# Performance work log

Hardware: AMD Instinct MI355X
Metric: run time of the kernel (lower is better)

## Reference

```python
import jax, jax.numpy as jnp
import numpy as np
import math

D_MODEL = 512
KEY_DIM = 128
NUM_LAYERS = 2
TEMP = 30.0
NORM_EPS = 1e-5
NORM_SCALE = math.sqrt(1.0 / (D_MODEL * 4 * 4))


def _l2norm_lastdim(x):
    # F.normalize(x, p=2, dim=-1): x / max(||x||, 1e-12)
    n = jnp.sqrt(jnp.sum(x * x, axis=-1, keepdims=True))
    return x / jnp.maximum(n, 1e-12)


def _attn(q, k, v, WK, bK):
    # q: [Sq,B,D], k: [Sk,B,D], v: [Sk,B,D] -> [Sq,B,D]
    wq = _l2norm_lastdim(q @ WK + bK)            # [Sq,B,K]
    wk = _l2norm_lastdim(k @ WK + bK)            # [Sk,B,K]
    dot = jnp.einsum('qbk,sbk->bqs', wq, wk)     # cosine sims
    aff = jax.nn.softmax(dot * TEMP, axis=-1)
    return jnp.einsum('bqs,sbd->qbd', aff, v)


def _instance_norm(x, h, w):
    # x: [HW,B,D]; InstanceL2Norm over (D,h,w) per batch element, size_average=True
    HW, B, D = x.shape
    ss = jnp.sum(x * x, axis=(0, 2))             # [B]
    factor = NORM_SCALE * jnp.sqrt((D * h * w) / (ss + NORM_EPS))
    return x * factor[None, :, None]


def _encoder(src4d, WKs, bKs):
    B, D, H, W = src4d.shape
    x = src4d.reshape(B, D, H * W).transpose(2, 0, 1)   # [HW,B,D]
    for _ in range(NUM_LAYERS):
        x = _instance_norm(x + _attn(x, x, x, WKs, bKs), H, W)
    return x  # memory [HW,B,D]


def _decoder(tgt4d, memory, pos, WKs, bKs, WKc, bKc):
    B, D, H, W = tgt4d.shape
    x = tgt4d.reshape(B, D, H * W).transpose(2, 0, 1)   # [HW,B,D]
    for _ in range(NUM_LAYERS):
        x = _instance_norm(x + _attn(x, x, x, WKs, bKs), H, W)
        mask = _attn(x, memory, pos, WKc, bKc)
        t2 = _instance_norm(x * mask, H, W)
        t3 = _attn(x, memory, memory * pos, WKc, bKc)
        t4 = _instance_norm(x + t3, H, W)
        x = _instance_norm(t2 + t4, H, W)
    feat = x.reshape(H, W, B, D).transpose(2, 3, 0, 1)  # [B,D,H,W]
    return feat


def setup_inputs() -> dict:
    key = jax.random.key(0)
    k1, k2, k3, k4, k5 = jax.random.split(key, 5)
    B, D, H, W = 16, D_MODEL, 32, 32
    std = math.sqrt(2.0 / KEY_DIM)
    return {
        'train_feat': jax.random.normal(k1, (B, D, H, W), jnp.float32),
        'test_feat': jax.random.normal(k2, (B, D, H, W), jnp.float32),
        'train_label': jax.random.uniform(k3, (B, H, W), jnp.float32),
        'WK_self': jax.random.normal(k4, (D, KEY_DIM), jnp.float32) * std,
        'bK_self': jnp.zeros((KEY_DIM,), jnp.float32),
        'WK_cross': jax.random.normal(k5, (D, KEY_DIM), jnp.float32) * std,
        'bK_cross': jnp.zeros((KEY_DIM,), jnp.float32),
    }


def reference(train_feat, test_feat, train_label, WK_self, bK_self, WK_cross, bK_cross):
    B, D, H, W = train_feat.shape
    memory = _encoder(train_feat, WK_self, bK_self)              # [HW,B,D]
    # pos: label [B,H,W] -> [HW,B,1] -> broadcast to [HW,B,D]
    pos = jnp.broadcast_to(train_label.reshape(B, H * W).T[:, :, None], (H * W, B, D))
    encoded_feat = _decoder(train_feat, memory, pos, WK_self, bK_self, WK_cross, bK_cross)
    decoded_feat = _decoder(test_feat, memory, pos, WK_self, bK_self, WK_cross, bK_cross)
    return (encoded_feat, decoded_feat)
```

## Files before the change

### kernel.cpp

```cpp
#include <hip/hip_runtime.h>
#include <math.h>

#define NB 16
#define SEQ 1024
#define DM 512
#define KD 128
#define TEMP_F 30.0f
#define NS_F 0.011048543456039805f
#define DS_F 524288.0f

#define SS_IDX(grp, b) (((grp) * NB + (b)) * 16)
#define SS_STRIDE 768
#define SS_STAGES 12
#define SS_FLOATS (SS_STRIDE * SS_STAGES)

typedef short bf16x8 __attribute__((ext_vector_type(8)));
typedef float f32x4 __attribute__((ext_vector_type(4)));
typedef unsigned short us;
typedef unsigned short us8 __attribute__((ext_vector_type(8)));

__device__ __forceinline__ us f2bf(float x) {
    union { float f; unsigned u; } v; v.f = x;
    unsigned r = v.u + 0x7fffu + ((v.u >> 16) & 1u);
    return (us)(r >> 16);
}
__device__ __forceinline__ float bf2f(us h) {
    union { unsigned u; float f; } v; v.u = ((unsigned)h) << 16;
    return v.f;
}

#define GLL16(gp, lp) __builtin_amdgcn_global_load_lds( \
    (__attribute__((address_space(1))) void*)(unsigned long long)(gp), \
    (__attribute__((address_space(3))) void*)(unsigned)(unsigned long long)(lp), 16, 0, 0)


__global__ __launch_bounds__(256) void k_transpose_in(const float* __restrict__ src,
                                                      us* __restrict__ XC,
                                                      us* __restrict__ XT) {
    __shared__ float tile[32][33];
    const int b = blockIdx.z;
    const int d0 = blockIdx.x * 32;
    const int s0 = blockIdx.y * 32;
    const int tx = threadIdx.x, ty = threadIdx.y;
    const float* p = src + (size_t)b * DM * SEQ;
    us* pt = XT + (size_t)b * DM * SEQ;
    us* pc = XC + (size_t)b * SEQ * 1024;
#pragma unroll
    for (int j = 0; j < 32; j += 8) {
        const size_t o = (size_t)(d0 + ty + j) * SEQ + s0 + tx;
        const float v = p[o];
        tile[ty + j][tx] = v;
        pt[o] = f2bf(v);
    }
    __syncthreads();
#pragma unroll
    for (int j = 0; j < 4; ++j) {
        const int s = s0 + ty + j * 8;
        const int d = d0 + tx;
        const float v = tile[tx][ty + j * 8];
        const us h = f2bf(v);
        pc[(size_t)s * 1024 + d] = h;
        pc[(size_t)s * 1024 + 512 + d] = f2bf(v - bf2f(h));
    }
}

__global__ __launch_bounds__(256) void k_mklabel(const us* __restrict__ MT,
                                                 const float* __restrict__ label,
                                                 us* __restrict__ ML) {
    const int b = blockIdx.y;
    const size_t off = ((size_t)blockIdx.x * 256 + threadIdx.x) * 8;
    const int s = (int)(off & (SEQ - 1));
    const size_t o = (size_t)b * DM * SEQ + off;
    us8 v = *(const us8*)(MT + o);
    const float4 l0 = *(const float4*)(label + (size_t)b * SEQ + s);
    const float4 l1 = *(const float4*)(label + (size_t)b * SEQ + s + 4);
    us8 r;
    r[0] = f2bf(bf2f(v[0]) * l0.x); r[1] = f2bf(bf2f(v[1]) * l0.y);
    r[2] = f2bf(bf2f(v[2]) * l0.z); r[3] = f2bf(bf2f(v[3]) * l0.w);
    r[4] = f2bf(bf2f(v[4]) * l1.x); r[5] = f2bf(bf2f(v[5]) * l1.y);
    r[6] = f2bf(bf2f(v[6]) * l1.z); r[7] = f2bf(bf2f(v[7]) * l1.w);
    *(us8*)(ML + o) = r;
}

__global__ __launch_bounds__(256) void k_wsplit(const float* __restrict__ WK,
                                                us* __restrict__ WC) {
    const int k = blockIdx.x;
    for (int d = threadIdx.x; d < DM; d += 256) {
        const float v = WK[(size_t)d * KD + k];
        const us h = f2bf(v);
        WC[(size_t)k * 1024 + d] = h;
        WC[(size_t)k * 1024 + 512 + d] = f2bf(v - bf2f(h));
    }
}

__global__ __launch_bounds__(256) void k_proj(const us* __restrict__ XC,
                                              const us* __restrict__ WC,
                                              const float* __restrict__ bK,
                                              us* __restrict__ Wout) {
    const int row0 = blockIdx.x * 32;
    __shared__ short As[32 * 64], Bs[128 * 64];
    __shared__ float ssp[2][32];
    const int tid = threadIdx.x, w = tid >> 6, l = tid & 63;
    const int wm = (w >> 1) * 16, wn = (w & 1) * 64;
    const int sr = l >> 3, sc = (((l & 7) ^ (l >> 3)) << 3);
    const int lr = l & 15, lk = (l >> 4) * 8;
    const int sx = (lr & 7) << 3;
    f32x4 acc[4] = {};
    for (int k0 = 0; k0 < 1536; k0 += 64) {
        const int ak0 = (k0 < 1024) ? k0 : k0 - 1024;
        const int bk0 = (k0 < 512) ? k0 : k0 - 512;
        GLL16(XC + (size_t)(row0 + w * 8 + sr) * 1024 + ak0 + sc, &As[w * 512]);
#pragma unroll
        for (int cc = 0; cc < 4; ++cc) {
            const int c = 4 * w + cc;
            GLL16(WC + (size_t)(c * 8 + sr) * 1024 + bk0 + sc, &Bs[c * 512]);
        }
        __syncthreads();
#pragma unroll
        for (int kc = 0; kc < 2; ++kc) {
            const int kk = kc * 32 + lk;
            const bf16x8 a = *(const bf16x8*)&As[(wm + lr) * 64 + (kk ^ sx)];
            bf16x8 bb[4];
#pragma unroll
            for (int fn = 0; fn < 4; ++fn)
                bb[fn] = *(const bf16x8*)&Bs[(wn + fn * 16 + lr) * 64 + (kk ^ sx)];
#pragma unroll
            for (int fn = 0; fn < 4; ++fn)
                acc[fn] = __builtin_amdgcn_mfma_f32_16x16x32_bf16(a, bb[fn], acc[fn], 0, 0, 0);
        }
        __syncthreads();
    }
    const int er = l & 15, eq = (l >> 4) * 4;
    const int nh = w & 1;
    float bkv[4];
#pragma unroll
    for (int fn = 0; fn < 4; ++fn) bkv[fn] = bK[wn + fn * 16 + er];
    float vv[4][4];
#pragma unroll
    for (int r = 0; r < 4; ++r) {
        float ss = 0.f;
#pragma unroll
        for (int fn = 0; fn < 4; ++fn) {
            const float t = acc[fn][r] + bkv[fn];
            vv[fn][r] = t;
            ss += t * t;
        }
#pragma unroll
        for (int o = 8; o > 0; o >>= 1) ss += __shfl_xor(ss, o, 64);
        if (er == 0) ssp[nh][wm + eq + r] = ss;
    }
    __syncthreads();
#pragma unroll
    for (int r = 0; r < 4; ++r) {
        const int rowloc = wm + eq + r;
        const float tot = ssp[0][rowloc] + ssp[1][rowloc];
        const float invn = 1.0f / fmaxf(sqrtf(tot), 1e-12f);
        const size_t ro = (size_t)(row0 + rowloc) * 256;
#pragma unroll
        for (int fn = 0; fn < 4; ++fn) {
            const float ov = vv[fn][r] * invn;
            const us h = f2bf(ov);
            Wout[ro + wn + fn * 16 + er] = h;
            Wout[ro + 128 + wn + fn * 16 + er] = f2bf(ov - bf2f(h));
        }
    }
}

__global__ __launch_bounds__(256) void k_qk(const us* __restrict__ Qc,
                                            const us* __restrict__ Kc,
                                            const float* __restrict__ labelp,
                                            us* __restrict__ P,
                                            float* __restrict__ RS,
                                            float* __restrict__ RL, int b0) {
    const int flat = blockIdx.x + (int)gridDim.x * (blockIdx.y + (int)gridDim.y * blockIdx.z);
    const int chunk = ((int)gridDim.x * (int)gridDim.y * (int)gridDim.z) >> 3;
    const int logical = (flat & 7) * chunk + (flat >> 3);
    const int jx = logical & 7;
    const int iy = (logical >> 3) & 7;
    const int bz = logical >> 6;
    const int b = b0 + bz;
    const int i0 = iy * 128, j0 = jx * 128;
    const int jb = jx;
    const us* Ab = Qc + (size_t)b * SEQ * 256;
    const us* Bb = Kc + (size_t)b * SEQ * 256;
    __shared__ short As[128 * 64], Bs[128 * 64];
    __shared__ float shrs[2][128], shrl[2][128];
    const int tid = threadIdx.x, w = tid >> 6, l = tid & 63;
    const int wm = (w >> 1) * 64, wn = (w & 1) * 64;
    const int sr = l >> 3, sc = (((l & 7) ^ (l >> 3)) << 3);
    const int lr = l & 15, lk = (l >> 4) * 8;
    const int sx = (lr & 7) << 3;
    f32x4 acc[4][4] = {};
    for (int k0 = 0; k0 < 384; k0 += 64) {
        const int ak0 = (k0 < 256) ? k0 : k0 - 256;
        const int bk0 = (k0 < 128) ? k0 : k0 - 128;
#pragma unroll
        for (int cc = 0; cc < 4; ++cc) {
            const int c = 4 * w + cc;
            GLL16(Ab + (size_t)(i0 + c * 8 + sr) * 256 + ak0 + sc, &As[c * 512]);
            GLL16(Bb + (size_t)(j0 + c * 8 + sr) * 256 + bk0 + sc, &Bs[c * 512]);
        }
        __syncthreads();
#pragma unroll
        for (int kc = 0; kc < 2; ++kc) {
            const int kk = kc * 32 + lk;
            bf16x8 a[4], bb[4];
#pragma unroll
            for (int f = 0; f < 4; ++f) {
                a[f]  = *(const bf16x8*)&As[(wm + f * 16 + lr) * 64 + (kk ^ sx)];
                bb[f] = *(const bf16x8*)&Bs[(wn + f * 16 + lr) * 64 + (kk ^ sx)];
            }
#pragma unroll
            for (int fm = 0; fm < 4; ++fm)
#pragma unroll
                for (int fn = 0; fn < 4; ++fn)
                    acc[fm][fn] = __builtin_amdgcn_mfma_f32_16x16x32_bf16(a[fm], bb[fn], acc[fm][fn], 0, 0, 0);
        }
        __syncthreads();
    }
    us* Pb = P + (size_t)bz * SEQ * SEQ;
    const int er = l & 15, eq = (l >> 4) * 4;
    float lb[4] = {0.f, 0.f, 0.f, 0.f};
    if (labelp) {
#pragma unroll
        for (int fn = 0; fn < 4; ++fn) lb[fn] = labelp[(size_t)b * SEQ + j0 + wn + fn * 16 + er];
    }
#pragma unroll
    for (int fm = 0; fm < 4; ++fm)
#pragma unroll
        for (int r = 0; r < 4; ++r) {
            float s = 0.f, sl = 0.f;
#pragma unroll
            for (int fn = 0; fn < 4; ++fn) {
                const float e = __expf(fmaf(TEMP_F, acc[fm][fn][r], -TEMP_F));
                Pb[(size_t)(i0 + wm + fm * 16 + eq + r) * SEQ + j0 + wn + fn * 16 + er] = f2bf(e);
                s += e;
                sl += e * lb[fn];
            }
#pragma unroll
            for (int o = 1; o < 16; o <<= 1) {
                s += __shfl_xor(s, o, 64);
                sl += __shfl_xor(sl, o, 64);
            }
            if (er == 0) {
                shrs[w & 1][wm + fm * 16 + eq + r] = s;
                shrl[w & 1][wm + fm * 16 + eq + r] = sl;
            }
        }
    __syncthreads();
    if (tid < 128) {
        const size_t o = ((size_t)b * 8 + jb) * SEQ + i0 + tid;
        RS[o] = shrs[0][tid] + shrs[1][tid];
        if (labelp) RL[o] = shrl[0][tid] + shrl[1][tid];
    }
}

__global__ __launch_bounds__(256) void k_pv(const us* __restrict__ P,
                                            const us* __restrict__ VT,
                                            const us* __restrict__ XC,
                                            const float* __restrict__ RS,
                                            const float* __restrict__ RL,
                                            float* __restrict__ MVEC,
                                            float* __restrict__ Cout,
                                            float* __restrict__ SS, int b0, int mode) {
    const int flat = blockIdx.x + (int)gridDim.x * (blockIdx.y + (int)gridDim.y * blockIdx.z);
    const int chunk = ((int)gridDim.x * (int)gridDim.y * (int)gridDim.z) >> 3;
    const int logical = (flat & 7) * chunk + (flat >> 3);
    const int jx = logical & 3;
    const int iy = (logical >> 2) & 15;
    const int bz = logical >> 6;
    const int b = b0 + bz;
    const int i0 = iy * 64, j0 = jx * 128;
    const us* Pb = P + (size_t)bz * SEQ * SEQ;
    const us* Vb = VT + (size_t)b * DM * SEQ;
    __shared__ short As[64 * 64], Bs[128 * 64];
    __shared__ float sh_inv[64], sh_m[64];
    __shared__ float ps[3][4];
    const int tid = threadIdx.x, w = tid >> 6, l = tid & 63;
    const int wm = (w >> 1) * 32, wn = (w & 1) * 64;
    const int sr = l >> 3, sc = (((l & 7) ^ (l >> 3)) << 3);
    const int lr = l & 15, lk = (l >> 4) * 8;
    const int sx = (lr & 7) << 3;
    f32x4 acc[2][4] = {};
    for (int k0 = 0; k0 < SEQ; k0 += 64) {
#pragma unroll
        for (int cc = 0; cc < 2; ++cc) {
            const int c = 2 * w + cc;
            GLL16(Pb + (size_t)(i0 + c * 8 + sr) * SEQ + k0 + sc, &As[c * 512]);
        }
#pragma unroll
        for (int cc = 0; cc < 4; ++cc) {
            const int c = 4 * w + cc;
            GLL16(Vb + (size_t)(j0 + c * 8 + sr) * SEQ + k0 + sc, &Bs[c * 512]);
        }
        __syncthreads();
#pragma unroll
        for (int kc = 0; kc < 2; ++kc) {
            const int kk = kc * 32 + lk;
            bf16x8 a[2], bb[4];
#pragma unroll
            for (int fm = 0; fm < 2; ++fm)
                a[fm] = *(const bf16x8*)&As[(wm + fm * 16 + lr) * 64 + (kk ^ sx)];
#pragma unroll
            for (int fn = 0; fn < 4; ++fn)
                bb[fn] = *(const bf16x8*)&Bs[(wn + fn * 16 + lr) * 64 + (kk ^ sx)];
#pragma unroll
            for (int fm = 0; fm < 2; ++fm)
#pragma unroll
                for (int fn = 0; fn < 4; ++fn)
                    acc[fm][fn] = __builtin_amdgcn_mfma_f32_16x16x32_bf16(a[fm], bb[fn], acc[fm][fn], 0, 0, 0);
        }
        __syncthreads();
    }
    if (tid < 64) {
        const size_t base = (size_t)b * 8 * SEQ + i0 + tid;
        float s = 0.f;
#pragma unroll
        for (int jb = 0; jb < 8; ++jb) s += RS[base + (size_t)jb * SEQ];
        const float inv = 1.0f / s;
        sh_inv[tid] = inv;
        if (mode == 2) {
            float sl = 0.f;
#pragma unroll
            for (int jb = 0; jb < 8; ++jb) sl += RL[base + (size_t)jb * SEQ];
            const float mv = sl * inv;
            sh_m[tid] = mv;
            if (jx == 0) MVEC[(size_t)b * SEQ + i0 + tid] = mv;
        }
    }
    __syncthreads();
    const us* XCb = XC + (size_t)b * SEQ * 1024;
    float sa = 0.f, sb = 0.f, sab = 0.f;
    const int er = l & 15, eq = (l >> 4) * 4;
#pragma unroll
    for (int fm = 0; fm < 2; ++fm)
#pragma unroll
        for (int fn = 0; fn < 4; ++fn)
#pragma unroll
            for (int r = 0; r < 4; ++r) {
                const int lrow = wm + fm * 16 + eq + r;
                const int col = j0 + wn + fn * 16 + er;
                float v = acc[fm][fn][r] * sh_inv[lrow];
                const size_t o = ((size_t)b * SEQ + i0 + lrow) * DM + col;
                const size_t xo = (size_t)(i0 + lrow) * 1024 + col;
                const float x = bf2f(XCb[xo]) + bf2f(XCb[xo + 512]);
                v += x;
                sb += v * v;
                if (mode == 2) {
                    const float a = x * sh_m[lrow];
                    sa += a * a;
                    sab += a * v;
                }
                Cout[o] = v;
            }
#pragma unroll
    for (int off = 32; off > 0; off >>= 1) {
        sb += __shfl_xor(sb, off, 64);
        if (mode == 2) { sa += __shfl_xor(sa, off, 64); sab += __shfl_xor(sab, off, 64); }
    }
    if (l == 0) { ps[0][w] = sb; ps[1][w] = sa; ps[2][w] = sab; }
    __syncthreads();
    if (tid == 0) {
        if (mode == 1) {
            atomicAdd(&SS[SS_IDX(0, b)], ps[0][0] + ps[0][1] + ps[0][2] + ps[0][3]);
        } else {
            atomicAdd(&SS[SS_IDX(0, b)], ps[1][0] + ps[1][1] + ps[1][2] + ps[1][3]);
            atomicAdd(&SS[SS_IDX(1, b)], ps[0][0] + ps[0][1] + ps[0][2] + ps[0][3]);
            atomicAdd(&SS[SS_IDX(2, b)], ps[2][0] + ps[2][1] + ps[2][2] + ps[2][3]);
        }
    }
}

__global__ void k_zero(float* __restrict__ SSb) {
    const int i = blockIdx.x * 256 + threadIdx.x;
    if (i < SS_FLOATS) SSb[i] = 0.0f;
}

__global__ __launch_bounds__(256) void k_finish(const float* __restrict__ Tin,
                                                const us* __restrict__ XCin,
                                                const float* __restrict__ mv,
                                                const float* __restrict__ SS,
                                                us* __restrict__ XCout,
                                                us* __restrict__ XTb,
                                                float* __restrict__ XTf,
                                                int mode, int writeXC) {
    const int b = blockIdx.z;
    const int s0 = blockIdx.x * 32, d0 = blockIdx.y * 32;
    const int tx = threadIdx.x, ty = threadIdx.y;
    __shared__ float tile[32][33];
    float f1 = 0.f, f2 = 0.f, f3;
    if (mode == 0) {
        f3 = NS_F * sqrtf(DS_F / (SS[SS_IDX(0, b)] + 1e-5f));
    } else {
        const float ssa = SS[SS_IDX(0, b)], ssb = SS[SS_IDX(1, b)], ssab = SS[SS_IDX(2, b)];
        f1 = NS_F * sqrtf(DS_F / (ssa + 1e-5f));
        f2 = NS_F * sqrtf(DS_F / (ssb + 1e-5f));
        const float ssc = f1 * f1 * ssa + 2.f * f1 * f2 * ssab + f2 * f2 * ssb;
        f3 = NS_F * sqrtf(DS_F / (ssc + 1e-5f));
    }
#pragma unroll
    for (int j = 0; j < 4; ++j) {
        const int s = s0 + ty + j * 8;
        const int d = d0 + tx;
        const size_t o = ((size_t)b * SEQ + s) * DM + d;
        const size_t xo = ((size_t)b * SEQ + s) * 1024 + d;
        float v;
        if (mode == 0) v = f3 * Tin[o];
        else {
            const float x = bf2f(XCin[xo]) + bf2f(XCin[xo + 512]);
            v = f3 * (f1 * x * mv[(size_t)b * SEQ + s] + f2 * Tin[o]);
        }
        if (writeXC) {
            const us h = f2bf(v);
            XCout[xo] = h;
            XCout[xo + 512] = f2bf(v - bf2f(h));
        }
        tile[ty + j * 8][tx] = v;
    }
    __syncthreads();
#pragma unroll
    for (int j = 0; j < 4; ++j) {
        const int d = d0 + ty + j * 8;
        const int s = s0 + tx;
        const float v = tile[tx][ty + j * 8];
        const size_t o = ((size_t)b * DM + d) * SEQ + s;
        if (XTb) XTb[o] = f2bf(v);
        else if (XTf) XTf[o] = v;
    }
}

extern "C" void kernel_launch(void* const* d_in, const int* in_sizes, int n_in,
                              void* d_out, int out_size, void* d_ws, size_t ws_size,
                              hipStream_t stream) {
    const float* train_feat = (const float*)d_in[0];
    const float* test_feat  = (const float*)d_in[1];
    const float* label      = (const float*)d_in[2];
    const float* WKs        = (const float*)d_in[3];
    const float* bKs        = (const float*)d_in[4];
    const float* WKc        = (const float*)d_in[5];
    const float* bKc        = (const float*)d_in[6];
    float* out = (float*)d_out;
    float* w = (float*)d_ws;

    const size_t SBD = (size_t)NB * SEQ * DM;
    const size_t SBK = (size_t)NB * SEQ * KD;

    float* T   = w;
    us* XC     = (us*)(T + SBD);
    us* XTd    = XC + 2 * SBD;
    us* MEMT   = XTd + SBD;
    us* MEMLT  = MEMT + SBD;
    us* W1C    = MEMLT + SBD;
    us* WKMC   = W1C + 2 * SBK;
    us* WCs    = WKMC + 2 * SBK;
    us* WCc    = WCs + (size_t)KD * 1024;
    float* MVEC = (float*)(WCc + (size_t)KD * 1024);
    float* SS   = MVEC + (size_t)NB * SEQ;
    float* RS   = SS + SS_FLOATS;
    float* RL   = RS + (size_t)NB * 8 * SEQ;
    float* Pf   = RL + (size_t)NB * 8 * SEQ;

    const size_t fixed = (size_t)(Pf - w);
    const size_t per = (size_t)SEQ * SEQ / 2;
    const size_t wsf = ws_size / 4;
    int cap = 1;
    if (wsf > fixed) {
        size_t c = (wsf - fixed) / per;
        if (c < 1) c = 1;
        if (c > NB) c = NB;
        cap = (int)c;
    }
    us* Pbuf = (us*)Pf;

    const dim3 gT_in(DM / 32, SEQ / 32, NB), bT(32, 8);
    const dim3 gFin(SEQ / 32, DM / 32, NB);

    int stage = 0;
    auto nextSS = [&]() { return SS + (size_t)(stage++) * SS_STRIDE; };

    auto attn = [&](const us* Qc, const us* Kc, const us* VT,
                    const float* labelp, int pvmode, float* SSst) {
        for (int b0 = 0; b0 < NB; b0 += cap) {
            const int nb = (NB - b0 < cap) ? NB - b0 : cap;
            k_qk<<<dim3(8, 8, nb), 256, 0, stream>>>(Qc, Kc, labelp, Pbuf, RS, RL, b0);
            k_pv<<<dim3(4, 16, nb), 256, 0, stream>>>(Pbuf, VT, XC, RS, RL, MVEC, T, SSst, b0, pvmode);
        }
    };

    k_zero<<<(SS_FLOATS + 255) / 256, 256, 0, stream>>>(SS);
    k_wsplit<<<KD, 256, 0, stream>>>(WKs, WCs);
    k_wsplit<<<KD, 256, 0, stream>>>(WKc, WCc);

    k_transpose_in<<<gT_in, bT, 0, stream>>>(train_feat, XC, MEMT);
    for (int l = 0; l < 2; ++l) {
        float* SSst = nextSS();
        k_proj<<<NB * SEQ / 32, 256, 0, stream>>>(XC, WCs, bKs, W1C);
        attn(W1C, W1C, MEMT, nullptr, 1, SSst);
        k_finish<<<gFin, bT, 0, stream>>>(T, XC, nullptr, SSst, XC, MEMT, nullptr, 0, 1);
    }
    k_proj<<<NB * SEQ / 32, 256, 0, stream>>>(XC, WCc, bKc, WKMC);
    k_mklabel<<<dim3(DM * SEQ / 8 / 256, NB), 256, 0, stream>>>(MEMT, label, MEMLT);

    auto decoder = [&](const float* feat, float* outp) {
        k_transpose_in<<<gT_in, bT, 0, stream>>>(feat, XC, XTd);
        for (int l = 0; l < 2; ++l) {
            float* SSst = nextSS();
            k_proj<<<NB * SEQ / 32, 256, 0, stream>>>(XC, WCs, bKs, W1C);
            attn(W1C, W1C, XTd, nullptr, 1, SSst);
            k_finish<<<gFin, bT, 0, stream>>>(T, XC, nullptr, SSst, XC, XTd, nullptr, 0, 1);
            float* SSst2 = nextSS();
            k_proj<<<NB * SEQ / 32, 256, 0, stream>>>(XC, WCc, bKc, W1C);
            attn(W1C, WKMC, MEMLT, label, 2, SSst2);
            if (l == 0)
                k_finish<<<gFin, bT, 0, stream>>>(T, XC, MVEC, SSst2, XC, XTd, nullptr, 1, 1);
            else
                k_finish<<<gFin, bT, 0, stream>>>(T, XC, MVEC, SSst2, XC, nullptr, outp, 1, 0);
        }
    };
    decoder(train_feat, out);
    decoder(test_feat, out + SBD);
}
```

Baseline: 1.013 ms.

## Fuse QK softmax and PV into single flash-style attention kernel

Replaces the two-kernel attention (QK writing a bf16 probability matrix to global memory, then PV reading it back) with one fused kernel per (batch, 64-query tile). The new kernel streams 32-key chunks of K and V through double-buffered LDS, computes exp scores, stages them in LDS as bf16 and accumulates the full 512-wide output in registers. Row sums and label sums are kept in registers, so the RS/RL buffers and batch chunking by workspace capacity go away. The intent is to remove the large P matrix round-trip through HBM and the extra launches. In exchange each block holds 128 accumulator floats per thread with occupancy of one block per CU, only 256 blocks are launched, and each block does small 32-key steps with a barrier per step.

```diff
diff --git a/kernel.cpp b/kernel.cpp
--- a/kernel.cpp
+++ b/kernel.cpp
@@ -166,193 +166,155 @@
     }
 }
 
-__global__ __launch_bounds__(256) void k_qk(const us* __restrict__ Qc,
-                                            const us* __restrict__ Kc,
-                                            const float* __restrict__ labelp,
-                                            us* __restrict__ P,
-                                            float* __restrict__ RS,
-                                            float* __restrict__ RL, int b0) {
-    const int flat = blockIdx.x + (int)gridDim.x * (blockIdx.y + (int)gridDim.y * blockIdx.z);
-    const int chunk = ((int)gridDim.x * (int)gridDim.y * (int)gridDim.z) >> 3;
-    const int logical = (flat & 7) * chunk + (flat >> 3);
-    const int jx = logical & 7;
-    const int iy = (logical >> 3) & 7;
-    const int bz = logical >> 6;
-    const int b = b0 + bz;
-    const int i0 = iy * 128, j0 = jx * 128;
-    const int jb = jx;
-    const us* Ab = Qc + (size_t)b * SEQ * 256;
-    const us* Bb = Kc + (size_t)b * SEQ * 256;
-    __shared__ short As[128 * 64], Bs[128 * 64];
-    __shared__ float shrs[2][128], shrl[2][128];
-    const int tid = threadIdx.x, w = tid >> 6, l = tid & 63;
-    const int wm = (w >> 1) * 64, wn = (w & 1) * 64;
-    const int sr = l >> 3, sc = (((l & 7) ^ (l >> 3)) << 3);
-    const int lr = l & 15, lk = (l >> 4) * 8;
-    const int sx = (lr & 7) << 3;
-    f32x4 acc[4][4] = {};
-    for (int k0 = 0; k0 < 384; k0 += 64) {
-        const int ak0 = (k0 < 256) ? k0 : k0 - 256;
-        const int bk0 = (k0 < 128) ? k0 : k0 - 128;
-#pragma unroll
-        for (int cc = 0; cc < 4; ++cc) {
-            const int c = 4 * w + cc;
-            GLL16(Ab + (size_t)(i0 + c * 8 + sr) * 256 + ak0 + sc, &As[c * 512]);
-            GLL16(Bb + (size_t)(j0 + c * 8 + sr) * 256 + bk0 + sc, &Bs[c * 512]);
-        }
-        __syncthreads();
-#pragma unroll
-        for (int kc = 0; kc < 2; ++kc) {
-            const int kk = kc * 32 + lk;
-            bf16x8 a[4], bb[4];
-#pragma unroll
-            for (int f = 0; f < 4; ++f) {
-                a[f]  = *(const bf16x8*)&As[(wm + f * 16 + lr) * 64 + (kk ^ sx)];
-                bb[f] = *(const bf16x8*)&Bs[(wn + f * 16 + lr) * 64 + (kk ^ sx)];
-            }
-#pragma unroll
-            for (int fm = 0; fm < 4; ++fm)
-#pragma unroll
-                for (int fn = 0; fn < 4; ++fn)
-                    acc[fm][fn] = __builtin_amdgcn_mfma_f32_16x16x32_bf16(a[fm], bb[fn], acc[fm][fn], 0, 0, 0);
-        }
-        __syncthreads();
-    }
-    us* Pb = P + (size_t)bz * SEQ * SEQ;
-    const int er = l & 15, eq = (l >> 4) * 4;
-    float lb[4] = {0.f, 0.f, 0.f, 0.f};
-    if (labelp) {
-#pragma unroll
-        for (int fn = 0; fn < 4; ++fn) lb[fn] = labelp[(size_t)b * SEQ + j0 + wn + fn * 16 + er];
-    }
-#pragma unroll
-    for (int fm = 0; fm < 4; ++fm)
-#pragma unroll
-        for (int r = 0; r < 4; ++r) {
-            float s = 0.f, sl = 0.f;
-#pragma unroll
-            for (int fn = 0; fn < 4; ++fn) {
-                const float e = __expf(fmaf(TEMP_F, acc[fm][fn][r], -TEMP_F));
-                Pb[(size_t)(i0 + wm + fm * 16 + eq + r) * SEQ + j0 + wn + fn * 16 + er] = f2bf(e);
-                s += e;
-                sl += e * lb[fn];
-            }
-#pragma unroll
-            for (int o = 1; o < 16; o <<= 1) {
-                s += __shfl_xor(s, o, 64);
-                sl += __shfl_xor(sl, o, 64);
-            }
-            if (er == 0) {
-                shrs[w & 1][wm + fm * 16 + eq + r] = s;
-                shrl[w & 1][wm + fm * 16 + eq + r] = sl;
-            }
-        }
-    __syncthreads();
-    if (tid < 128) {
-        const size_t o = ((size_t)b * 8 + jb) * SEQ + i0 + tid;
-        RS[o] = shrs[0][tid] + shrs[1][tid];
-        if (labelp) RL[o] = shrl[0][tid] + shrl[1][tid];
-    }
-}
-
-__global__ __launch_bounds__(256) void k_pv(const us* __restrict__ P,
-                                            const us* __restrict__ VT,
-                                            const us* __restrict__ XC,
-                                            const float* __restrict__ RS,
-                                            const float* __restrict__ RL,
-                                            float* __restrict__ MVEC,
-                                            float* __restrict__ Cout,
-                                            float* __restrict__ SS, int b0, int mode) {
-    const int flat = blockIdx.x + (int)gridDim.x * (blockIdx.y + (int)gridDim.y * blockIdx.z);
-    const int chunk = ((int)gridDim.x * (int)gridDim.y * (int)gridDim.z) >> 3;
-    const int logical = (flat & 7) * chunk + (flat >> 3);
-    const int jx = logical & 3;
-    const int iy = (logical >> 2) & 15;
-    const int bz = logical >> 6;
-    const int b = b0 + bz;
-    const int i0 = iy * 64, j0 = jx * 128;
-    const us* Pb = P + (size_t)bz * SEQ * SEQ;
-    const us* Vb = VT + (size_t)b * DM * SEQ;
-    __shared__ short As[64 * 64], Bs[128 * 64];
-    __shared__ float sh_inv[64], sh_m[64];
+__global__ __launch_bounds__(256, 1) void k_attn(const us* __restrict__ Qc,
+                                                 const us* __restrict__ Kc,
+                                                 const us* __restrict__ VT,
+                                                 const us* __restrict__ XC,
+                                                 const float* __restrict__ labelp,
+                                                 float* __restrict__ MVEC,
+                                                 float* __restrict__ Cout,
+                                                 float* __restrict__ SS, int mode) {
+    const int b = blockIdx.x;
+    const int q0 = blockIdx.y * 64;
+    __shared__ short QL[4 * 64 * 64];
+    __shared__ short KL[2][4 * 32 * 64];
+    __shared__ short VL[2][512 * 32];
+    __shared__ us PL[4 * 16 * 40];
+    __shared__ float LBL[1024];
     __shared__ float ps[3][4];
     const int tid = threadIdx.x, w = tid >> 6, l = tid & 63;
-    const int wm = (w >> 1) * 32, wn = (w & 1) * 64;
-    const int sr = l >> 3, sc = (((l & 7) ^ (l >> 3)) << 3);
+    const us* Qb = Qc + (size_t)b * SEQ * 256;
+    const us* Kb = Kc + (size_t)b * SEQ * 256;
+    const us* Vb = VT + (size_t)b * DM * SEQ;
+
+#pragma unroll
+    for (int i = 0; i < 8; ++i) {
+        const int c = w * 8 + i, rg = c >> 2, p = c & 3;
+        GLL16(Qb + (size_t)(q0 + rg * 8 + (l >> 3)) * 256 + p * 64 + (((l & 7) ^ (l >> 3)) << 3),
+              &QL[p * 4096 + rg * 512 + l * 8]);
+    }
+#pragma unroll
+    for (int i = 0; i < 1; ++i) {
+        const int c = w, rg = c >> 2, p = c & 3;
+        GLL16(Kb + (size_t)(rg * 8 + (l >> 3)) * 256 + p * 64 + (((l & 7) ^ (l >> 3)) << 3),
+              &KL[0][p * 2048 + rg * 512 + l * 8]);
+    }
+#pragma unroll
+    for (int i = 0; i < 3; ++i) {
+        const int c = 4 + w * 3 + i, rg = c >> 2, p = c & 3;
+        GLL16(Kb + (size_t)(rg * 8 + (l >> 3)) * 256 + p * 64 + (((l & 7) ^ (l >> 3)) << 3),
+              &KL[0][p * 2048 + rg * 512 + l * 8]);
+    }
+#pragma unroll
+    for (int i = 0; i < 8; ++i) {
+        const int c = w * 8 + i;
+        GLL16(Vb + (size_t)(c * 16 + (l >> 2)) * SEQ + ((((l & 3) ^ ((l >> 2) & 3))) << 3),
+              &VL[0][c * 512 + l * 8]);
+    }
+    if (labelp) {
+        GLL16(labelp + (size_t)b * SEQ + w * 256 + l * 4, &LBL[w * 256 + l * 4]);
+    }
+    __syncthreads();
+
     const int lr = l & 15, lk = (l >> 4) * 8;
-    const int sx = (lr & 7) << 3;
-    f32x4 acc[2][4] = {};
-    for (int k0 = 0; k0 < SEQ; k0 += 64) {
-#pragma unroll
-        for (int cc = 0; cc < 2; ++cc) {
-            const int c = 2 * w + cc;
-            GLL16(Pb + (size_t)(i0 + c * 8 + sr) * SEQ + k0 + sc, &As[c * 512]);
-        }
-#pragma unroll
-        for (int cc = 0; cc < 4; ++cc) {
-            const int c = 4 * w + cc;
-            GLL16(Vb + (size_t)(j0 + c * 8 + sr) * SEQ + k0 + sc, &Bs[c * 512]);
+    const int sx = (l & 7) << 3;
+    const int vx = (l & 3) << 3;
+    f32x4 acc[32];
+#pragma unroll
+    for (int i = 0; i < 32; ++i) acc[i] = (f32x4){0.f, 0.f, 0.f, 0.f};
+    float rsum[4] = {0.f, 0.f, 0.f, 0.f}, rlsum[4] = {0.f, 0.f, 0.f, 0.f};
+    us* PLw = &PL[w * 640];
+    int cur = 0;
+    for (int it = 0; it < 32; ++it) {
+        if (it < 31) {
+            const int s1 = (it + 1) * 32;
+            const int nb2 = cur ^ 1;
+#pragma unroll
+            for (int i = 0; i < 4; ++i) {
+                const int c = w * 4 + i, rg = c >> 2, p = c & 3;
+                GLL16(Kb + (size_t)(s1 + rg * 8 + (l >> 3)) * 256 + p * 64 + (((l & 7) ^ (l >> 3)) << 3),
+                      &KL[nb2][p * 2048 + rg * 512 + l * 8]);
+            }
+#pragma unroll
+            for (int i = 0; i < 8; ++i) {
+                const int c = w * 8 + i;
+                GLL16(Vb + (size_t)(c * 16 + (l >> 2)) * SEQ + s1 + ((((l & 3) ^ ((l >> 2) & 3))) << 3),
+                      &VL[nb2][c * 512 + l * 8]);
+            }
+        }
+        f32x4 sacc[2] = {};
+#pragma unroll
+        for (int kc = 0; kc < 12; ++kc) {
+            const int vk = kc * 32;
+            const int ak0 = (vk < 256) ? vk : vk - 256;
+            const int bk0 = (vk < 128) ? vk : vk - 128;
+            const int ca = (ak0 & 63) + lk, cb = (bk0 & 63) + lk;
+            const bf16x8 a = *(const bf16x8*)&QL[(ak0 >> 6) * 4096 + (w * 16 + lr) * 64 + (ca ^ sx)];
+#pragma unroll
+            for (int sn = 0; sn < 2; ++sn) {
+                const bf16x8 bb = *(const bf16x8*)&KL[cur][(bk0 >> 6) * 2048 + (sn * 16 + lr) * 64 + (cb ^ sx)];
+                sacc[sn] = __builtin_amdgcn_mfma_f32_16x16x32_bf16(a, bb, sacc[sn], 0, 0, 0);
+            }
+        }
+        const int s0 = it * 32;
+#pragma unroll
+        for (int sn = 0; sn < 2; ++sn)
+#pragma unroll
+            for (int r = 0; r < 4; ++r) {
+                const float e = __expf(fmaf(TEMP_F, sacc[sn][r], -TEMP_F));
+                const int q = (l >> 4) * 4 + r;
+                const int s = sn * 16 + lr;
+                rsum[r] += e;
+                if (mode == 2) rlsum[r] += e * LBL[s0 + s];
+                PLw[q * 40 + s] = f2bf(e);
+            }
+        const bf16x8 pa = *(const bf16x8*)&PLw[lr * 40 + lk];
+#pragma unroll
+        for (int fn = 0; fn < 32; ++fn) {
+            const int d = fn * 16 + lr;
+            const bf16x8 vb = *(const bf16x8*)&VL[cur][d * 32 + (lk ^ vx)];
+            acc[fn] = __builtin_amdgcn_mfma_f32_16x16x32_bf16(pa, vb, acc[fn], 0, 0, 0);
         }
         __syncthreads();
-#pragma unroll
-        for (int kc = 0; kc < 2; ++kc) {
-            const int kk = kc * 32 + lk;
-            bf16x8 a[2], bb[4];
-#pragma unroll
-            for (int fm = 0; fm < 2; ++fm)
-                a[fm] = *(const bf16x8*)&As[(wm + fm * 16 + lr) * 64 + (kk ^ sx)];
-#pragma unroll
-            for (int fn = 0; fn < 4; ++fn)
-                bb[fn] = *(const bf16x8*)&Bs[(wn + fn * 16 + lr) * 64 + (kk ^ sx)];
-#pragma unroll
-            for (int fm = 0; fm < 2; ++fm)
-#pragma unroll
-                for (int fn = 0; fn < 4; ++fn)
-                    acc[fm][fn] = __builtin_amdgcn_mfma_f32_16x16x32_bf16(a[fm], bb[fn], acc[fm][fn], 0, 0, 0);
-        }
-        __syncthreads();
-    }
-    if (tid < 64) {
-        const size_t base = (size_t)b * 8 * SEQ + i0 + tid;
-        float s = 0.f;
-#pragma unroll
-        for (int jb = 0; jb < 8; ++jb) s += RS[base + (size_t)jb * SEQ];
-        const float inv = 1.0f / s;
-        sh_inv[tid] = inv;
-        if (mode == 2) {
-            float sl = 0.f;
-#pragma unroll
-            for (int jb = 0; jb < 8; ++jb) sl += RL[base + (size_t)jb * SEQ];
-            const float mv = sl * inv;
-            sh_m[tid] = mv;
-            if (jx == 0) MVEC[(size_t)b * SEQ + i0 + tid] = mv;
-        }
-    }
-    __syncthreads();
+        cur ^= 1;
+    }
+
+#pragma unroll
+    for (int o = 1; o < 16; o <<= 1)
+#pragma unroll
+        for (int r = 0; r < 4; ++r) {
+            rsum[r] += __shfl_xor(rsum[r], o, 64);
+            rlsum[r] += __shfl_xor(rlsum[r], o, 64);
+        }
+    float inv[4], mv[4];
+#pragma unroll
+    for (int r = 0; r < 4; ++r) {
+        inv[r] = 1.0f / rsum[r];
+        mv[r] = rlsum[r] * inv[r];
+    }
+    const int qbase = q0 + w * 16 + (l >> 4) * 4;
+    if (mode == 2 && lr == 0) {
+#pragma unroll
+        for (int r = 0; r < 4; ++r)
+            MVEC[(size_t)b * SEQ + qbase + r] = mv[r];
+    }
     const us* XCb = XC + (size_t)b * SEQ * 1024;
     float sa = 0.f, sb = 0.f, sab = 0.f;
-    const int er = l & 15, eq = (l >> 4) * 4;
-#pragma unroll
-    for (int fm = 0; fm < 2; ++fm)
-#pragma unroll
-        for (int fn = 0; fn < 4; ++fn)
-#pragma unroll
-            for (int r = 0; r < 4; ++r) {
-                const int lrow = wm + fm * 16 + eq + r;
-                const int col = j0 + wn + fn * 16 + er;
-                float v = acc[fm][fn][r] * sh_inv[lrow];
-                const size_t o = ((size_t)b * SEQ + i0 + lrow) * DM + col;
-                const size_t xo = (size_t)(i0 + lrow) * 1024 + col;
-                const float x = bf2f(XCb[xo]) + bf2f(XCb[xo + 512]);
-                v += x;
-                sb += v * v;
-                if (mode == 2) {
-                    const float a = x * sh_m[lrow];
-                    sa += a * a;
-                    sab += a * v;
-                }
-                Cout[o] = v;
-            }
+#pragma unroll
+    for (int fn = 0; fn < 32; ++fn)
+#pragma unroll
+        for (int r = 0; r < 4; ++r) {
+            const int row = qbase + r;
+            const int col = fn * 16 + lr;
+            float v = acc[fn][r] * inv[r];
+            const size_t o = ((size_t)b * SEQ + row) * DM + col;
+            const size_t xo = (size_t)row * 1024 + col;
+            const float x = bf2f(XCb[xo]) + bf2f(XCb[xo + 512]);
+            v += x;
+            sb += v * v;
+            if (mode == 2) { const float a = x * mv[r]; sa += a * a; sab += a * v; }
+            Cout[o] = v;
+        }
 #pragma unroll
     for (int off = 32; off > 0; off >>= 1) {
         sb += __shfl_xor(sb, off, 64);
@@ -456,36 +418,13 @@
     us* WCc    = WCs + (size_t)KD * 1024;
     float* MVEC = (float*)(WCc + (size_t)KD * 1024);
     float* SS   = MVEC + (size_t)NB * SEQ;
-    float* RS   = SS + SS_FLOATS;
-    float* RL   = RS + (size_t)NB * 8 * SEQ;
-    float* Pf   = RL + (size_t)NB * 8 * SEQ;
-
-    const size_t fixed = (size_t)(Pf - w);
-    const size_t per = (size_t)SEQ * SEQ / 2;
-    const size_t wsf = ws_size / 4;
-    int cap = 1;
-    if (wsf > fixed) {
-        size_t c = (wsf - fixed) / per;
-        if (c < 1) c = 1;
-        if (c > NB) c = NB;
-        cap = (int)c;
-    }
-    us* Pbuf = (us*)Pf;
 
     const dim3 gT_in(DM / 32, SEQ / 32, NB), bT(32, 8);
     const dim3 gFin(SEQ / 32, DM / 32, NB);
+    const dim3 gAtt(NB, SEQ / 64);
 
     int stage = 0;
     auto nextSS = [&]() { return SS + (size_t)(stage++) * SS_STRIDE; };
-
-    auto attn = [&](const us* Qc, const us* Kc, const us* VT,
-                    const float* labelp, int pvmode, float* SSst) {
-        for (int b0 = 0; b0 < NB; b0 += cap) {
-            const int nb = (NB - b0 < cap) ? NB - b0 : cap;
-            k_qk<<<dim3(8, 8, nb), 256, 0, stream>>>(Qc, Kc, labelp, Pbuf, RS, RL, b0);
-            k_pv<<<dim3(4, 16, nb), 256, 0, stream>>>(Pbuf, VT, XC, RS, RL, MVEC, T, SSst, b0, pvmode);
-        }
-    };
 
     k_zero<<<(SS_FLOATS + 255) / 256, 256, 0, stream>>>(SS);
     k_wsplit<<<KD, 256, 0, stream>>>(WKs, WCs);
@@ -495,7 +434,7 @@
     for (int l = 0; l < 2; ++l) {
         float* SSst = nextSS();
         k_proj<<<NB * SEQ / 32, 256, 0, stream>>>(XC, WCs, bKs, W1C);
-        attn(W1C, W1C, MEMT, nullptr, 1, SSst);
+        k_attn<<<gAtt, 256, 0, stream>>>(W1C, W1C, MEMT, XC, nullptr, nullptr, T, SSst, 1);
         k_finish<<<gFin, bT, 0, stream>>>(T, XC, nullptr, SSst, XC, MEMT, nullptr, 0, 1);
     }
     k_proj<<<NB * SEQ / 32, 256, 0, stream>>>(XC, WCc, bKc, WKMC);
@@ -506,11 +445,11 @@
         for (int l = 0; l < 2; ++l) {
             float* SSst = nextSS();
             k_proj<<<NB * SEQ / 32, 256, 0, stream>>>(XC, WCs, bKs, W1C);
-            attn(W1C, W1C, XTd, nullptr, 1, SSst);
+            k_attn<<<gAtt, 256, 0, stream>>>(W1C, W1C, XTd, XC, nullptr, nullptr, T, SSst, 1);
             k_finish<<<gFin, bT, 0, stream>>>(T, XC, nullptr, SSst, XC, XTd, nullptr, 0, 1);
             float* SSst2 = nextSS();
             k_proj<<<NB * SEQ / 32, 256, 0, stream>>>(XC, WCc, bKc, W1C);
-            attn(W1C, WKMC, MEMLT, label, 2, SSst2);
+            k_attn<<<gAtt, 256, 0, stream>>>(W1C, WKMC, MEMLT, XC, label, MVEC, T, SSst2, 2);
             if (l == 0)
                 k_finish<<<gFin, bT, 0, stream>>>(T, XC, MVEC, SSst2, XC, XTd, nullptr, 1, 1);
             else
```

Measured after the change: 1.099 ms. +8.5%, slower.
